# Performance work log

Hardware: AMD Instinct MI355X
Metric: run time of the kernel (lower is better)

The kernel has to match this reference:

```python
import jax, jax.numpy as jnp
import numpy as np

D_MODEL = 1024
HEADS = 16
D_K = D_MODEL // HEADS


def setup_inputs() -> dict:
    key = jax.random.key(0)
    ks = jax.random.split(key, 11)
    bs, seq = 2, 2048
    scale = 1.0 / np.sqrt(D_MODEL)
    inp = {
        "query": jax.random.normal(ks[0], (bs, seq, D_MODEL), jnp.float32),
        "key": jax.random.normal(ks[1], (bs, seq, D_MODEL), jnp.float32),
        "value": jax.random.normal(ks[2], (bs, seq, D_MODEL), jnp.float32),
        # nn.Linear weights: y = x @ W.T + b, W shape [out, in]
        "Wq": jax.random.normal(ks[3], (D_MODEL, D_MODEL), jnp.float32) * scale,
        "bq": jnp.zeros((D_MODEL,), jnp.float32),
        "Wk": jax.random.normal(ks[4], (D_MODEL, D_MODEL), jnp.float32) * scale,
        "bk": jnp.zeros((D_MODEL,), jnp.float32),
        "Wv": jax.random.normal(ks[5], (D_MODEL, D_MODEL), jnp.float32) * scale,
        "bv": jnp.zeros((D_MODEL,), jnp.float32),
        "Wo": jax.random.normal(ks[6], (D_MODEL, D_MODEL), jnp.float32) * scale,
        "bo": jnp.zeros((D_MODEL,), jnp.float32),
    }
    return inp


def _split_heads(x, bs):
    # [b, s, d_model] -> [b, h, s, d_k]
    return x.reshape(bs, -1, HEADS, D_K).transpose(0, 2, 1, 3)


def reference(query, key, value, Wq, bq, Wk, bk, Wv, bv, Wo, bo):
    bs = query.shape[0]
    q = _split_heads(query @ Wq.T + bq, bs)
    k = _split_heads(key @ Wk.T + bk, bs)
    v = _split_heads(value @ Wv.T + bv, bs)
    # scaled dot-product attention (dropout is identity at eval)
    logits = jnp.einsum("bhqd,bhkd->bhqk", q, k) / np.sqrt(D_K).astype(np.float32)
    probs = jax.nn.softmax(logits, axis=-1)
    scores = jnp.einsum("bhqk,bhkd->bhqd", probs, v)  # [b, h, s, d_k]
    concat = scores.transpose(0, 2, 1, 3).reshape(bs, -1, D_MODEL)
    output = concat @ Wo.T + bo
    return (output, scores)
```

## Files before the change

### kernel.cpp

```cpp
#include <hip/hip_runtime.h>
#include <stdint.h>
#include <math.h>

typedef __bf16 bf16;
typedef __bf16 bf16x4 __attribute__((ext_vector_type(4)));
typedef __bf16 bf16x8 __attribute__((ext_vector_type(8)));
typedef float floatx4 __attribute__((ext_vector_type(4)));
typedef float floatx16 __attribute__((ext_vector_type(16)));

#define CEXP 0.1803368801111204f

typedef __attribute__((address_space(1))) const void gvoid_t;
typedef __attribute__((address_space(3))) void lvoid_t;
#define GLOAD_LDS16(g, l) \
  __builtin_amdgcn_global_load_lds((gvoid_t*)(g), (lvoid_t*)(l), 16, 0, 0)

__global__ __launch_bounds__(256) void wcvt_kernel(
    const float* __restrict__ Wq, const float* __restrict__ Wk,
    const float* __restrict__ Wv, const float* __restrict__ Wo,
    bf16* __restrict__ dst)
{
  const float* src = (blockIdx.y == 0) ? Wq : (blockIdx.y == 1) ? Wk
                   : (blockIdx.y == 2) ? Wv : Wo;
  bf16* d = dst + (size_t)blockIdx.y * 1048576;
  const int i = (blockIdx.x * 256 + threadIdx.x) * 4;
  const floatx4 v = *(const floatx4*)(src + i);
  bf16x4 o;
#pragma unroll
  for (int j = 0; j < 4; ++j) o[j] = (bf16)v[j];
  *(bf16x4*)(d + i) = o;
}

__global__ __launch_bounds__(256) void xcvt_kernel(
    const float* __restrict__ q, const float* __restrict__ k,
    const float* __restrict__ v,
    bf16* __restrict__ Qb, bf16* __restrict__ Kb, bf16* __restrict__ Vb)
{
  const float* src = (blockIdx.y == 0) ? q : (blockIdx.y == 1) ? k : v;
  bf16* d = (blockIdx.y == 0) ? Qb : (blockIdx.y == 1) ? Kb : Vb;
  const int i = (blockIdx.x * 256 + threadIdx.x) * 4;
  const floatx4 val = *(const floatx4*)(src + i);
  bf16x4 o;
#pragma unroll
  for (int j = 0; j < 4; ++j) o[j] = (bf16)val[j];
  *(bf16x4*)(d + i) = o;
}

__device__ __forceinline__ void gemm_body(
    const bf16* __restrict__ Ab,
    const bf16* __restrict__ Wb, const float* __restrict__ bias,
    void* __restrict__ Cout, const int mode, const float oscale)
{
  __shared__ __align__(16) char smem[36864];

  const int tid  = threadIdx.x;
  const int wave = tid >> 6;
  const int lane = tid & 63;
  const int mlane = lane & 15;
  const int quad  = lane >> 4;
  const int m0 = blockIdx.x * 128;
  const int n0 = blockIdx.y * 128;
  const int wm = (wave >> 1) * 64;
  const int wn = (wave & 1) * 64;

  const int srow8 = tid >> 3;
  const int ch    = tid & 7;

  auto stage = [&](int k0) {
    bf16* Abuf = (bf16*)smem;
    bf16* Bbuf = (bf16*)(smem + 16384);
#pragma unroll
    for (int i = 0; i < 4; ++i) {
      const int row = i * 32 + srow8;
      const bf16* ga;
      if (mode == 1) {
        const int token = m0 + row;
        const int bb = token >> 11, s = token & 2047;
        const int h = k0 >> 6;
        ga = Ab + (((size_t)(bb * 16 + h) * 2048 + s) << 6) + ch * 8;
      } else {
        ga = Ab + (size_t)(m0 + row) * 1024 + k0 + ch * 8;
      }
      GLOAD_LDS16(ga, Abuf + i * 2048 + wave * 512);
      const bf16* gb = Wb + (size_t)(n0 + row) * 1024 + k0 + ch * 8;
      GLOAD_LDS16(gb, Bbuf + i * 2048 + wave * 512);
    }
  };

  floatx4 acc[4][4] = {};

  for (int k0 = 0; k0 < 1024; k0 += 64) {
    stage(k0);
    __syncthreads();

    const bf16* As = (const bf16*)smem;
    const bf16* Bs = (const bf16*)(smem + 16384);
#pragma unroll
    for (int kk = 0; kk < 64; kk += 32) {
      bf16x8 af[4], bfr[4];
#pragma unroll
      for (int t = 0; t < 4; ++t) {
        af[t]  = *(const bf16x8*)&As[(wm + t * 16 + mlane) * 64 + kk + quad * 8];
        bfr[t] = *(const bf16x8*)&Bs[(wn + t * 16 + mlane) * 64 + kk + quad * 8];
      }
#pragma unroll
      for (int mt = 0; mt < 4; ++mt)
#pragma unroll
        for (int nt = 0; nt < 4; ++nt)
          acc[mt][nt] = __builtin_amdgcn_mfma_f32_16x16x32_bf16(
              af[mt], bfr[nt], acc[mt][nt], 0, 0, 0);
    }
    __syncthreads();
  }

  if (mode == 2) {
    bf16* T = (bf16*)smem + wave * 4608;
#pragma unroll
    for (int nt = 0; nt < 4; ++nt) {
      const float bv = bias[n0 + wn + nt * 16 + mlane];
#pragma unroll
      for (int mt = 0; mt < 4; ++mt) {
        bf16x4 t4;
#pragma unroll
        for (int r = 0; r < 4; ++r)
          t4[r] = (bf16)((acc[mt][nt][r] + bv) * oscale);
        *(bf16x4*)&T[(nt * 16 + mlane) * 72 + mt * 16 + quad * 4] = t4;
      }
    }
    asm volatile("s_waitcnt lgkmcnt(0)" ::: "memory");
    const int token0 = m0 + wm;
    const int bb = token0 >> 11;
    const int srow0 = token0 & 2047;
    const int h = (n0 + wn) >> 6;
    const int dl = lane >> 3;
    const int s8 = (lane & 7) * 8;
    bf16* outp = (bf16*)Cout + ((size_t)(bb * 16 + h) << 17);
#pragma unroll
    for (int p = 0; p < 8; ++p) {
      const int dk = p * 8 + dl;
      const bf16x8 v8 = *(const bf16x8*)&T[dk * 72 + s8];
      *(bf16x8*)&outp[((size_t)dk << 11) + srow0 + s8] = v8;
    }
    return;
  }

#pragma unroll
  for (int nt = 0; nt < 4; ++nt) {
    const int col = n0 + wn + nt * 16 + mlane;
    const float bv = bias[col];
#pragma unroll
    for (int mt = 0; mt < 4; ++mt) {
#pragma unroll
      for (int r = 0; r < 4; ++r) {
        const int row = m0 + wm + mt * 16 + quad * 4 + r;
        const float v = (acc[mt][nt][r] + bv) * oscale;
        if (mode == 0) {
          const int b = row >> 11, s = row & 2047;
          const int h = col >> 6, dk = col & 63;
          ((bf16*)Cout)[(((size_t)(b * 16 + h) * 2048 + s) << 6) + dk] = (bf16)v;
        } else {
          ((float*)Cout)[(size_t)row * 1024 + col] = v;
        }
      }
    }
  }
}

__global__ __launch_bounds__(256) void qkv_kernel(
    const bf16* __restrict__ Qb, const bf16* __restrict__ Kb,
    const bf16* __restrict__ Vb, const bf16* __restrict__ Wb,
    const float* __restrict__ bq, const float* __restrict__ bk,
    const float* __restrict__ bv,
    bf16* __restrict__ Qw, bf16* __restrict__ Kw, bf16* __restrict__ Vw)
{
  const int z = blockIdx.z;
  const bf16* A = (z == 0) ? Qb : (z == 1) ? Kb : Vb;
  const bf16* W = Wb + (size_t)z * 1048576;
  const float* B = (z == 0) ? bq : (z == 1) ? bk : bv;
  if (z == 2)      gemm_body(A, W, B, Vw, 2, 1.0f);
  else if (z == 1) gemm_body(A, W, B, Kw, 0, 1.0f);
  else             gemm_body(A, W, B, Qw, 0, CEXP);
}

__global__ __launch_bounds__(256) void out_kernel(
    const bf16* __restrict__ Sb, const bf16* __restrict__ Wob,
    const float* __restrict__ bo, float* __restrict__ out)
{
  gemm_body(Sb, Wob, bo, out, 1, 1.0f);
}

__global__ __launch_bounds__(256, 2) void attn_kernel(
    const bf16* __restrict__ Qw, const bf16* __restrict__ Kw,
    const bf16* __restrict__ Vtg, float* __restrict__ scores,
    bf16* __restrict__ Sb)
{
  __shared__ __align__(16) char smem[2 * 2 * 64 * 136];

  const int tid  = threadIdx.x;
  const int wave = tid >> 6;
  const int lane = tid & 63;
  const int c    = lane & 31;
  const int hi   = lane >> 5;

  const int g = blockIdx.x + (blockIdx.y << 4);
  const int slot = g >> 3;
  const int bh = ((g & 7) << 2) + (slot >> 4);
  const int q0 = (slot & 15) << 7;
  const size_t base = (size_t)bh << 17;

  const int srow = tid >> 2;
  const int sce  = (tid & 3) * 16;

  bf16x8 qf[4];
#pragma unroll
  for (int m = 0; m < 4; ++m)
    qf[m] = *(const bf16x8*)
        &Qw[base + (size_t)(q0 + wave * 32 + c) * 64 + m * 16 + hi * 8];

  floatx16 o[2] = {};
  float rs = 0.f;

  bf16x8 kpf[2], vpf[2];
  auto load_kv = [&](int kt) {
    const bf16* kp = &Kw[base + (size_t)(kt + srow) * 64 + sce];
    kpf[0] = *(const bf16x8*)kp;
    kpf[1] = *(const bf16x8*)(kp + 8);
    const bf16* vp = &Vtg[base + (size_t)srow * 2048 + kt + sce];
    vpf[0] = *(const bf16x8*)vp;
    vpf[1] = *(const bf16x8*)(vp + 8);
  };
  auto stage = [&](int b) {
    char* kr = smem + b * 17408 + srow * 136 + (tid & 3) * 32;
    char* vr = kr + 8704;
    *(bf16x4*)(kr +  0) = ((const bf16x4*)&kpf[0])[0];
    *(bf16x4*)(kr +  8) = ((const bf16x4*)&kpf[0])[1];
    *(bf16x4*)(kr + 16) = ((const bf16x4*)&kpf[1])[0];
    *(bf16x4*)(kr + 24) = ((const bf16x4*)&kpf[1])[1];
    *(bf16x4*)(vr +  0) = ((const bf16x4*)&vpf[0])[0];
    *(bf16x4*)(vr +  8) = ((const bf16x4*)&vpf[0])[1];
    *(bf16x4*)(vr + 16) = ((const bf16x4*)&vpf[1])[0];
    *(bf16x4*)(vr + 24) = ((const bf16x4*)&vpf[1])[1];
  };

  load_kv(0);
  stage(0);
  load_kv(64);
  __syncthreads();

  for (int kt = 0; kt < 2048; kt += 64) {
    const int cur = (kt >> 6) & 1;
    if (kt + 64 < 2048) {
      stage(cur ^ 1);
      if (kt + 128 < 2048) load_kv(kt + 128);
    }
    const char* KsB = smem + cur * 17408;
    const char* VsB = KsB + 8704;

#pragma unroll
    for (int ks = 0; ks < 2; ++ks) {
      const char* krow = KsB + (ks * 32 + c) * 136;
      floatx16 s = {};
      __builtin_amdgcn_s_setprio(1);
#pragma unroll
      for (int m = 0; m < 4; ++m) {
        bf16x8 a;
        ((bf16x4*)&a)[0] = *(const bf16x4*)(krow + m * 32 + hi * 16);
        ((bf16x4*)&a)[1] = *(const bf16x4*)(krow + m * 32 + hi * 16 + 8);
        s = __builtin_amdgcn_mfma_f32_32x32x16_bf16(a, qf[m], s, 0, 0, 0);
      }
      __builtin_amdgcn_s_setprio(0);

      float p[16];
#pragma unroll
      for (int i = 0; i < 16; ++i) p[i] = __builtin_amdgcn_exp2f(s[i]);
#pragma unroll
      for (int i = 0; i < 16; ++i) rs += p[i];

      uint32_t ulo[4], uhi[4];
#pragma unroll
      for (int gg = 0; gg < 4; ++gg) {
        asm("v_cvt_pk_bf16_f32 %0, %1, %2"
            : "=v"(ulo[gg]) : "v"(p[4 * gg]), "v"(p[4 * gg + 1]));
        asm("v_cvt_pk_bf16_f32 %0, %1, %2"
            : "=v"(uhi[gg]) : "v"(p[4 * gg + 2]), "v"(p[4 * gg + 3]));
      }

      __builtin_amdgcn_s_setprio(1);
#pragma unroll
      for (int t = 0; t < 2; ++t) {
        uint32_t w0 = ulo[2 * t], w2 = ulo[2 * t + 1];
        uint32_t w1 = uhi[2 * t], w3 = uhi[2 * t + 1];
        asm("v_permlane32_swap_b32 %0, %1" : "+v"(w0), "+v"(w2));
        asm("v_permlane32_swap_b32 %0, %1" : "+v"(w1), "+v"(w3));
        union { bf16x8 v; uint32_t w[4]; } pu;
        pu.w[0] = w0; pu.w[1] = w1; pu.w[2] = w2; pu.w[3] = w3;
#pragma unroll
        for (int d = 0; d < 2; ++d) {
          const char* vrow = VsB + (d * 32 + c) * 136 + ks * 64 + t * 32 + hi * 16;
          bf16x8 va;
          ((bf16x4*)&va)[0] = *(const bf16x4*)(vrow);
          ((bf16x4*)&va)[1] = *(const bf16x4*)(vrow + 8);
          o[d] = __builtin_amdgcn_mfma_f32_32x32x16_bf16(va, pu.v, o[d], 0, 0, 0);
        }
      }
      __builtin_amdgcn_s_setprio(0);
    }
    __syncthreads();
  }

  rs += __shfl_xor(rs, 32, 64);
  const float inv = 1.0f / rs;

  const int q = q0 + wave * 32 + c;
  float* sr = scores + base + (size_t)q * 64;
  bf16*  br = Sb + base + (size_t)q * 64;
#pragma unroll
  for (int d = 0; d < 2; ++d)
#pragma unroll
    for (int gg = 0; gg < 4; ++gg) {
      const int dk = d * 32 + gg * 8 + hi * 4;
      floatx4 v4;
      bf16x4 b4;
#pragma unroll
      for (int i = 0; i < 4; ++i) {
        const float v = o[d][gg * 4 + i] * inv;
        v4[i] = v;
        b4[i] = (bf16)v;
      }
      *(floatx4*)(sr + dk) = v4;
      *(bf16x4*)(br + dk) = b4;
    }
}

extern "C" void kernel_launch(void* const* d_in, const int* in_sizes, int n_in,
                              void* d_out, int out_size, void* d_ws, size_t ws_size,
                              hipStream_t stream) {
  const float* query = (const float*)d_in[0];
  const float* key   = (const float*)d_in[1];
  const float* value = (const float*)d_in[2];
  const float* Wq = (const float*)d_in[3];
  const float* bq = (const float*)d_in[4];
  const float* Wk = (const float*)d_in[5];
  const float* bk = (const float*)d_in[6];
  const float* Wv = (const float*)d_in[7];
  const float* bv = (const float*)d_in[8];
  const float* Wo = (const float*)d_in[9];
  const float* bo = (const float*)d_in[10];

  float* out    = (float*)d_out;
  float* scores = out + (size_t)4194304;

  bf16* Wb  = (bf16*)d_ws;
  bf16* Qws = Wb  + (size_t)4194304;
  bf16* Kws = Qws + (size_t)4194304;
  bf16* Vws = Kws + (size_t)4194304;
  bf16* Sb  = Vws + (size_t)4194304;

  bf16* Qb = (bf16*)out;
  bf16* Kb = Qb + (size_t)4194304;
  bf16* Vb = (bf16*)scores;

  wcvt_kernel<<<dim3(1024, 4), 256, 0, stream>>>(Wq, Wk, Wv, Wo, Wb);
  xcvt_kernel<<<dim3(4096, 3), 256, 0, stream>>>(query, key, value, Qb, Kb, Vb);
  qkv_kernel<<<dim3(32, 8, 3), 256, 0, stream>>>(Qb, Kb, Vb, Wb,
                                                 bq, bk, bv, Qws, Kws, Vws);
  attn_kernel<<<dim3(16, 32), 256, 0, stream>>>(Qws, Kws, Vws, scores, Sb);
  out_kernel<<<dim3(32, 8), 256, 0, stream>>>(Sb, Wb + (size_t)3145728, bo, out);
}
```

Measured before the change: 238.0 us.

## Pre-swizzle bf16 operands in global memory to avoid LDS bank conflicts

The weight and activation conversion kernels are merged into one launch, and each thread now converts 8 elements and writes them at an XOR-swizzled 16-byte chunk position within each 1024-wide row. The attention kernel writes its bf16 scores copy with the same swizzle. Because global_load_lds copies data straight into LDS without rearranging it, the GEMM fragment reads apply a matching XOR to their column index, which is meant to remove LDS bank conflicts on the MFMA operand loads. The cost is more index arithmetic, and correctness depends on every producer and consumer using the same swizzle, including the head-split mode-1 path.

Measured after the change: 223.3 us. 1.07x faster.

```diff
diff --git a/kernel.cpp b/kernel.cpp
--- a/kernel.cpp
+++ b/kernel.cpp
@@ -15,35 +15,35 @@
 #define GLOAD_LDS16(g, l) \
   __builtin_amdgcn_global_load_lds((gvoid_t*)(g), (lvoid_t*)(l), 16, 0, 0)
 
-__global__ __launch_bounds__(256) void wcvt_kernel(
+__global__ __launch_bounds__(256) void cvt_kernel(
     const float* __restrict__ Wq, const float* __restrict__ Wk,
     const float* __restrict__ Wv, const float* __restrict__ Wo,
-    bf16* __restrict__ dst)
-{
-  const float* src = (blockIdx.y == 0) ? Wq : (blockIdx.y == 1) ? Wk
-                   : (blockIdx.y == 2) ? Wv : Wo;
-  bf16* d = dst + (size_t)blockIdx.y * 1048576;
-  const int i = (blockIdx.x * 256 + threadIdx.x) * 4;
-  const floatx4 v = *(const floatx4*)(src + i);
-  bf16x4 o;
-#pragma unroll
-  for (int j = 0; j < 4; ++j) o[j] = (bf16)v[j];
-  *(bf16x4*)(d + i) = o;
-}
-
-__global__ __launch_bounds__(256) void xcvt_kernel(
-    const float* __restrict__ q, const float* __restrict__ k,
+    const float* __restrict__ q,  const float* __restrict__ k,
     const float* __restrict__ v,
-    bf16* __restrict__ Qb, bf16* __restrict__ Kb, bf16* __restrict__ Vb)
-{
-  const float* src = (blockIdx.y == 0) ? q : (blockIdx.y == 1) ? k : v;
-  bf16* d = (blockIdx.y == 0) ? Qb : (blockIdx.y == 1) ? Kb : Vb;
-  const int i = (blockIdx.x * 256 + threadIdx.x) * 4;
-  const floatx4 val = *(const floatx4*)(src + i);
-  bf16x4 o;
-#pragma unroll
-  for (int j = 0; j < 4; ++j) o[j] = (bf16)val[j];
-  *(bf16x4*)(d + i) = o;
+    bf16* __restrict__ Wb, bf16* __restrict__ Qb,
+    bf16* __restrict__ Kb, bf16* __restrict__ Vb)
+{
+  const int y = blockIdx.y;
+  const float* src;
+  bf16* dst;
+  if (y < 4) {
+    if (blockIdx.x >= 512) return;
+    src = (y == 0) ? Wq : (y == 1) ? Wk : (y == 2) ? Wv : Wo;
+    dst = Wb + (size_t)y * 1048576;
+  } else {
+    src = (y == 4) ? q : (y == 5) ? k : v;
+    dst = (y == 4) ? Qb : (y == 5) ? Kb : Vb;
+  }
+  const int i   = blockIdx.x * 256 + threadIdx.x;
+  const int row = i >> 7;
+  const int cl  = i & 127;
+  const int dc  = (cl & ~7) | ((cl ^ row) & 7);
+  const floatx4 v0 = *(const floatx4*)(src + (size_t)i * 8);
+  const floatx4 v1 = *(const floatx4*)(src + (size_t)i * 8 + 4);
+  bf16x8 o;
+#pragma unroll
+  for (int j = 0; j < 4; ++j) { o[j] = (bf16)v0[j]; o[4 + j] = (bf16)v1[j]; }
+  *(bf16x8*)(dst + (size_t)row * 1024 + dc * 8) = o;
 }
 
 __device__ __forceinline__ void gemm_body(
@@ -88,6 +88,7 @@
   };
 
   floatx4 acc[4][4] = {};
+  const int swz = mlane & 7;
 
   for (int k0 = 0; k0 < 1024; k0 += 64) {
     stage(k0);
@@ -97,11 +98,12 @@
     const bf16* Bs = (const bf16*)(smem + 16384);
 #pragma unroll
     for (int kk = 0; kk < 64; kk += 32) {
+      const int cidx = ((quad + (kk >> 3)) ^ swz) << 3;
       bf16x8 af[4], bfr[4];
 #pragma unroll
       for (int t = 0; t < 4; ++t) {
-        af[t]  = *(const bf16x8*)&As[(wm + t * 16 + mlane) * 64 + kk + quad * 8];
-        bfr[t] = *(const bf16x8*)&Bs[(wn + t * 16 + mlane) * 64 + kk + quad * 8];
+        af[t]  = *(const bf16x8*)&As[(wm + t * 16 + mlane) * 64 + cidx];
+        bfr[t] = *(const bf16x8*)&Bs[(wn + t * 16 + mlane) * 64 + cidx];
       }
 #pragma unroll
       for (int mt = 0; mt < 4; ++mt)
@@ -312,6 +314,7 @@
   const float inv = 1.0f / rs;
 
   const int q = q0 + wave * 32 + c;
+  const int ssw = c & 7;
   float* sr = scores + base + (size_t)q * 64;
   bf16*  br = Sb + base + (size_t)q * 64;
 #pragma unroll
@@ -319,6 +322,7 @@
 #pragma unroll
     for (int gg = 0; gg < 4; ++gg) {
       const int dk = d * 32 + gg * 8 + hi * 4;
+      const int dks = (((d * 4 + gg) ^ ssw) << 3) + hi * 4;
       floatx4 v4;
       bf16x4 b4;
 #pragma unroll
@@ -328,7 +332,7 @@
         b4[i] = (bf16)v;
       }
       *(floatx4*)(sr + dk) = v4;
-      *(bf16x4*)(br + dk) = b4;
+      *(bf16x4*)(br + dks) = b4;
     }
 }
 
@@ -360,8 +364,9 @@
   bf16* Kb = Qb + (size_t)4194304;
   bf16* Vb = (bf16*)scores;
 
-  wcvt_kernel<<<dim3(1024, 4), 256, 0, stream>>>(Wq, Wk, Wv, Wo, Wb);
-  xcvt_kernel<<<dim3(4096, 3), 256, 0, stream>>>(query, key, value, Qb, Kb, Vb);
+  cvt_kernel<<<dim3(2048, 7), 256, 0, stream>>>(Wq, Wk, Wv, Wo,
+                                                query, key, value,
+                                                Wb, Qb, Kb, Vb);
   qkv_kernel<<<dim3(32, 8, 3), 256, 0, stream>>>(Qb, Kb, Vb, Wb,
                                                  bq, bk, bv, Qws, Kws, Vws);
   attn_kernel<<<dim3(16, 32), 256, 0, stream>>>(Qws, Kws, Vws, scores, Sb);
```
